# Kernel optimization log

Measured on AMD Instinct MI355X. Metric: run time of the kernel, lower is better.

The kernel has to match this reference:

```python
import jax, jax.numpy as jnp
import numpy as np

K = 20
EPS = 1e-5
NEG_SLOPE = 0.2


def knn_idx(x, k):
    # x: (B, C, N) -> idx: (B, N, k) of nearest neighbors by L2 distance
    inner = jnp.einsum('bcn,bcm->bnm', x, x)          # (B, N, N)
    xx = jnp.sum(x * x, axis=1)                        # (B, N)
    # negative squared distance: larger = closer
    neg_dist = 2.0 * inner - xx[:, :, None] - xx[:, None, :]
    _, idx = jax.lax.top_k(neg_dist, k)                # (B, N, k)
    return idx


def edge_feature(x, k):
    # x: (B, C, N) -> (B, 2C, N, k): concat(neighbor - x, x)
    idx = knn_idx(x, k)                                # (B, N, k)
    # neighbors[b,c,n,j] = x[b, c, idx[b,n,j]]
    nbr = jnp.take_along_axis(x[:, :, None, :], idx[:, None, :, :], axis=3)  # (B,C,N,k)
    xc = x[:, :, :, None]
    return jnp.concatenate([nbr - xc, jnp.broadcast_to(xc, nbr.shape)], axis=1)


def conv_bn_lrelu(h, W, gamma, beta):
    # 1x1 conv: h (B, Cin, N, k), W (Cout, Cin)
    h = jnp.einsum('oc,bcnk->bonk', W, h)
    # training-mode BatchNorm2d over (B, N, k) per channel
    mean = jnp.mean(h, axis=(0, 2, 3), keepdims=True)
    var = jnp.var(h, axis=(0, 2, 3), keepdims=True)
    h = (h - mean) * jax.lax.rsqrt(var + EPS)
    h = h * gamma[None, :, None, None] + beta[None, :, None, None]
    return jnp.where(h >= 0, h, NEG_SLOPE * h)


def setup_inputs() -> dict:
    key = jax.random.key(0)
    ks = jax.random.split(key, 3)
    B, C, N = 16, 3, 4096
    x = jax.random.normal(ks[0], (B, C, N), dtype=jnp.float32)
    W0 = jax.random.normal(ks[1], (64, 2 * C), dtype=jnp.float32) * (1.0 / np.sqrt(2 * C))
    W1 = jax.random.normal(ks[2], (64, 64), dtype=jnp.float32) * (1.0 / np.sqrt(64))
    g0 = jnp.ones((64,), jnp.float32); b0 = jnp.zeros((64,), jnp.float32)
    g1 = jnp.ones((64,), jnp.float32); b1 = jnp.zeros((64,), jnp.float32)
    return {"x": x, "W0": W0, "g0": g0, "b0": b0, "W1": W1, "g1": g1, "b1": b1}


def reference(x, W0, g0, b0, W1, g1, b1):
    h = edge_feature(x, K)                 # (B, 2C, N, k)
    h = conv_bn_lrelu(h, W0, g0, b0)       # (B, 64, N, k)
    h = conv_bn_lrelu(h, W1, g1, b1)       # (B, 64, N, k)
    return jnp.max(h, axis=-1)             # (B, 64, N)
```

## Files before the change

### kernel.cpp

```cpp
#include <hip/hip_runtime.h>
#include <cfloat>

#define NEG_SLOPE 0.2f
#define BN_EPS 1e-5f
#define EDGES 1310720
#define INV_M (1.0f / 1310720.0f)

typedef short v8s __attribute__((ext_vector_type(8)));
typedef float v4f __attribute__((ext_vector_type(4)));

__device__ __forceinline__ unsigned short f2bf(float f) {
  unsigned b = __float_as_uint(f);
  b += 0x7fffu + ((b >> 16) & 1u);
  return (unsigned short)(b >> 16);
}
__device__ __forceinline__ float bf2f(unsigned short s) {
  return __uint_as_float(((unsigned)s) << 16);
}

__device__ __forceinline__ float sqnorm_np(float c0, float c1, float c2) {
#pragma clang fp contract(off)
  return (c0 * c0 + c1 * c1) + c2 * c2;
}
__device__ __forceinline__ float negdist_np(float c0, float c1, float c2,
                                            float q0, float q1, float q2,
                                            float xxn, float xxm) {
#pragma clang fp contract(off)
  float inner = (c0 * q0 + c1 * q1) + c2 * q2;
  return (2.0f * inner - xxn) - xxm;
}

template <int PAT>
__device__ __forceinline__ float swzf(float v) {
  return __uint_as_float((unsigned)__builtin_amdgcn_ds_swizzle((int)__float_as_uint(v), PAT));
}
template <int PAT>
__device__ __forceinline__ int swzi(int v) {
  return __builtin_amdgcn_ds_swizzle(v, PAT);
}
__device__ __forceinline__ float bpermf(int addr, float v) {
  return __uint_as_float((unsigned)__builtin_amdgcn_ds_bpermute(addr, (int)__float_as_uint(v)));
}
__device__ __forceinline__ int bpermi(int addr, int v) {
  return __builtin_amdgcn_ds_bpermute(addr, v);
}
__device__ __forceinline__ int imin2(int a, int b) { return a < b ? a : b; }

__device__ __forceinline__ int pick_max(float v0, int i0, int xaddr) {
  float m = fmaxf(v0, swzf<0x041F>(v0));
  m = fmaxf(m, swzf<0x081F>(m));
  m = fmaxf(m, swzf<0x101F>(m));
  m = fmaxf(m, swzf<0x201F>(m));
  m = fmaxf(m, swzf<0x401F>(m));
  float vmax = fmaxf(m, bpermf(xaddr, m));
  unsigned long long mask = __ballot(v0 == vmax);
  if (__popcll(mask) == 1) {
    int L = (int)(__ffsll(mask) - 1);
    return __builtin_amdgcn_readlane(i0, L);
  }
  int t = (v0 == vmax) ? i0 : 0x7fffffff;
  t = imin2(t, swzi<0x041F>(t));
  t = imin2(t, swzi<0x081F>(t));
  t = imin2(t, swzi<0x101F>(t));
  t = imin2(t, swzi<0x201F>(t));
  t = imin2(t, swzi<0x401F>(t));
  t = imin2(t, bpermi(xaddr, t));
  return t;
}

__device__ __forceinline__ void ins3f(float nd, int m,
                                      float& v0, float& v1, float& v2,
                                      int& i0, int& i1, int& i2) {
  bool g0 = nd > v0, g1 = nd > v1, g2 = nd > v2;
  int ni2 = g2 ? (g1 ? i1 : m) : i2;
  int ni1 = g1 ? (g0 ? i0 : m) : i1;
  i0 = g0 ? m : i0;
  float nv1 = __builtin_amdgcn_fmed3f(nd, v0, v1);
  float nv2 = __builtin_amdgcn_fmed3f(nd, v1, v2);
  v0 = fmaxf(v0, nd);
  v1 = nv1; v2 = nv2; i1 = ni1; i2 = ni2;
}

__global__ __launch_bounds__(1024, 8) void k1_knn(const float* __restrict__ x, int* __restrict__ idxo) {
  __shared__ float4 xs[4096];
  int b   = blockIdx.x >> 5;
  int blk = blockIdx.x & 31;
  const float* xb = x + b * 12288;
  for (int i = threadIdx.x; i < 4096; i += 1024) {
    float a0 = xb[i], a1 = xb[4096 + i], a2 = xb[8192 + i];
    xs[i] = make_float4(a0, a1, a2, sqnorm_np(a0, a1, a2));
  }
  __syncthreads();

  int wv = threadIdx.x >> 6;
  int lane = threadIdx.x & 63;
  int wave_id = blk * 16 + wv;
  int xaddr = ((lane ^ 32) << 2);

  #pragma unroll 1
  for (int p = 0; p < 4; p++) {
    int nA = wave_id * 8 + 2 * p;
    int nB = nA + 1;
    float4 qA = xs[nA];
    float4 qB = xs[nB];

    float vA0 = -FLT_MAX, vA1 = -FLT_MAX, vA2 = -FLT_MAX;
    float vB0 = -FLT_MAX, vB1 = -FLT_MAX, vB2 = -FLT_MAX;
    int   iA0 = 0x7fffffff, iA1 = 0x7fffffff, iA2 = 0x7fffffff;
    int   iB0 = 0x7fffffff, iB1 = 0x7fffffff, iB2 = 0x7fffffff;
    #pragma unroll 2
    for (int j = 0; j < 64; j++) {
      int m = (j << 6) + lane;
      float4 c = xs[m];
      float ndA = negdist_np(c.x, c.y, c.z, qA.x, qA.y, qA.z, qA.w, c.w);
      ins3f(ndA, m, vA0, vA1, vA2, iA0, iA1, iA2);
      float ndB = negdist_np(c.x, c.y, c.z, qB.x, qB.y, qB.z, qB.w, c.w);
      ins3f(ndB, m, vB0, vB1, vB2, iB0, iB1, iB2);
    }

    unsigned long long remA = 0ull, remB = 0ull;
    int keepA = 0, keepB = 0;
    #pragma unroll 1
    for (int r = 0; r < 20; r++) {
      int winA = pick_max(vA0, iA0, xaddr);
      int winB = pick_max(vB0, iB0, xaddr);
      if (lane == r) { keepA = winA; keepB = winB; }

      bool ownA = ((winA & 63) == lane);
      remA |= ownA ? (1ull << (winA >> 6)) : 0ull;
      vA0 = ownA ? vA1 : vA0;  iA0 = ownA ? iA1 : iA0;
      vA1 = ownA ? vA2 : vA1;  iA1 = ownA ? iA2 : iA1;
      vA2 = ownA ? -FLT_MAX : vA2;  iA2 = ownA ? 0x7fffffff : iA2;
      if (ownA & (vA0 == -FLT_MAX)) {
        #pragma unroll 1
        for (int j = 0; j < 64; j++) {
          int m = (j << 6) + lane;
          float4 c = xs[m];
          float ndA = negdist_np(c.x, c.y, c.z, qA.x, qA.y, qA.z, qA.w, c.w);
          if ((remA >> j) & 1ull) ndA = -FLT_MAX;
          ins3f(ndA, m, vA0, vA1, vA2, iA0, iA1, iA2);
        }
      }
      bool ownB = ((winB & 63) == lane);
      remB |= ownB ? (1ull << (winB >> 6)) : 0ull;
      vB0 = ownB ? vB1 : vB0;  iB0 = ownB ? iB1 : iB0;
      vB1 = ownB ? vB2 : vB1;  iB1 = ownB ? iB2 : iB1;
      vB2 = ownB ? -FLT_MAX : vB2;  iB2 = ownB ? 0x7fffffff : iB2;
      if (ownB & (vB0 == -FLT_MAX)) {
        #pragma unroll 1
        for (int j = 0; j < 64; j++) {
          int m = (j << 6) + lane;
          float4 c = xs[m];
          float ndB = negdist_np(c.x, c.y, c.z, qB.x, qB.y, qB.z, qB.w, c.w);
          if ((remB >> j) & 1ull) ndB = -FLT_MAX;
          ins3f(ndB, m, vB0, vB1, vB2, iB0, iB1, iB2);
        }
      }
    }
    if (lane < 20) {
      idxo[((b << 12) + nA) * 20 + lane] = keepA;
      idxo[((b << 12) + nB) * 20 + lane] = keepB;
    }
  }
}

__global__ __launch_bounds__(256) void k2_moments(const float* __restrict__ x,
                                                  const int* __restrict__ idxi,
                                                  float* __restrict__ stat) {
  int P = blockIdx.x * 256 + threadIdx.x;
  int b = P >> 12, n = P & 4095;
  const float* xb = x + b * 12288;
  float xn0 = xb[n], xn1 = xb[4096 + n], xn2 = xb[8192 + n];
  const int* ip = idxi + P * 20;
  float Sd0 = 0.f, Sd1 = 0.f, Sd2 = 0.f;
  float S00 = 0.f, S01 = 0.f, S02 = 0.f, S11 = 0.f, S12 = 0.f, S22 = 0.f;
  #pragma unroll 4
  for (int j = 0; j < 20; j++) {
    int m = ip[j];
    float d0 = xb[m] - xn0, d1 = xb[4096 + m] - xn1, d2 = xb[8192 + m] - xn2;
    Sd0 += d0; Sd1 += d1; Sd2 += d2;
    S00 = fmaf(d0, d0, S00); S01 = fmaf(d0, d1, S01); S02 = fmaf(d0, d2, S02);
    S11 = fmaf(d1, d1, S11); S12 = fmaf(d1, d2, S12); S22 = fmaf(d2, d2, S22);
  }
  float acc[27];
  acc[0] = Sd0; acc[1] = Sd1; acc[2] = Sd2;
  acc[3] = 20.f * xn0; acc[4] = 20.f * xn1; acc[5] = 20.f * xn2;
  acc[6] = S00;  acc[7] = S01;  acc[8] = S02;
  acc[9] = Sd0 * xn0;  acc[10] = Sd0 * xn1; acc[11] = Sd0 * xn2;
  acc[12] = S11; acc[13] = S12;
  acc[14] = Sd1 * xn0; acc[15] = Sd1 * xn1; acc[16] = Sd1 * xn2;
  acc[17] = S22;
  acc[18] = Sd2 * xn0; acc[19] = Sd2 * xn1; acc[20] = Sd2 * xn2;
  acc[21] = 20.f * xn0 * xn0; acc[22] = 20.f * xn0 * xn1; acc[23] = 20.f * xn0 * xn2;
  acc[24] = 20.f * xn1 * xn1; acc[25] = 20.f * xn1 * xn2;
  acc[26] = 20.f * xn2 * xn2;
  #pragma unroll
  for (int i = 0; i < 27; i++) {
    float s = acc[i];
    for (int off = 32; off > 0; off >>= 1) s += __shfl_down(s, off);
    acc[i] = s;
  }
  __shared__ float red[4][27];
  int w = threadIdx.x >> 6, lane = threadIdx.x & 63;
  if (lane == 0) {
    #pragma unroll
    for (int i = 0; i < 27; i++) red[w][i] = acc[i];
  }
  __syncthreads();
  if (threadIdx.x < 27) {
    float s = red[0][threadIdx.x] + red[1][threadIdx.x] + red[2][threadIdx.x] + red[3][threadIdx.x];
    atomicAdd(&stat[threadIdx.x], s);
  }
}

__global__ __launch_bounds__(256) void k0_uv(const float* __restrict__ x, const float* __restrict__ W0,
                                             const float* __restrict__ stat,
                                             const float* __restrict__ g0v, const float* __restrict__ b0v,
                                             unsigned short* __restrict__ u, unsigned short* __restrict__ v) {
  int gid = blockIdx.x * 256 + threadIdx.x;
  int p = gid >> 6;
  int c = gid & 63;
  int b = p >> 12, n = p & 4095;

  float w[6];
  #pragma unroll
  for (int i = 0; i < 6; i++) w[i] = W0[c * 6 + i];
  float mean = 0.f;
  #pragma unroll
  for (int i = 0; i < 6; i++) mean += w[i] * stat[i];
  mean *= INV_M;
  float e2 = 0.f;
  int pp = 6;
  #pragma unroll
  for (int i = 0; i < 6; i++) {
    #pragma unroll
    for (int j = i; j < 6; j++) {
      float f = w[i] * w[j] * stat[pp]; pp++;
      e2 += (i == j) ? f : 2.f * f;
    }
  }
  e2 *= INV_M;
  float var = e2 - mean * mean;
  float a = g0v[c] * rsqrtf(var + BN_EPS);
  float bb = b0v[c] - mean * a;

  const float* xb = x + b * 12288;
  float x0 = xb[n], x1 = xb[4096 + n], x2 = xb[8192 + n];
  float uu = a * (w[0] * x0 + w[1] * x1 + w[2] * x2);
  float vv = a * ((w[3] - w[0]) * x0 + (w[4] - w[1]) * x1 + (w[5] - w[2]) * x2) + bb;
  u[gid] = f2bf(uu);
  v[gid] = f2bf(vv);
}

__global__ __launch_bounds__(256, 4) void k4_mfma(const unsigned short* __restrict__ u,
                                                  const unsigned short* __restrict__ v,
                                                  const int* __restrict__ idxi,
                                                  const float* __restrict__ W1,
                                                  float* __restrict__ psum,
                                                  unsigned short* __restrict__ maxb,
                                                  unsigned short* __restrict__ minb) {
  int lane = threadIdx.x & 63;
  int wv = threadIdx.x >> 6;
  int g = blockIdx.x * 4 + wv;
  int G = g * 16;
  int bbase = (G >> 12) << 12;
  int row16 = lane & 15;
  int quad = lane >> 4;

  v8s Bf[4][2];
  #pragma unroll
  for (int t = 0; t < 4; t++) {
    const float* wrow = W1 + (16 * t + row16) * 64 + quad * 8;
    #pragma unroll
    for (int kh = 0; kh < 2; kh++) {
      #pragma unroll
      for (int i = 0; i < 8; i++) Bf[t][kh][i] = (short)f2bf(wrow[kh * 32 + i]);
    }
  }
  const v8s* vrow = (const v8s*)(v + (G + row16) * 64);
  v8s vv0 = vrow[quad], vv1 = vrow[quad + 4];
  float v0f[8], v1f[8];
  #pragma unroll
  for (int i = 0; i < 8; i++) {
    v0f[i] = bf2f((unsigned short)vv0[i]);
    v1f[i] = bf2f((unsigned short)vv1[i]);
  }

  const int* ip = idxi + (G + row16) * 20;

  float mx[4][4], mn[4][4], s2a[4], sq2a[4];
  #pragma unroll
  for (int t = 0; t < 4; t++) {
    #pragma unroll
    for (int i = 0; i < 4; i++) { mx[t][i] = -FLT_MAX; mn[t][i] = FLT_MAX; }
    s2a[t] = 0.f; sq2a[t] = 0.f;
  }

  int m_next = ip[0];
  #pragma unroll 1
  for (int j = 0; j < 20; j++) {
    int m = bbase + m_next;
    if (j < 19) m_next = ip[j + 1];
    const v8s* urow = (const v8s*)(u + m * 64);
    v8s u0 = urow[quad], u1 = urow[quad + 4];
    v8s a0, a1f;
    #pragma unroll
    for (int i = 0; i < 8; i++) {
      float h = bf2f((unsigned short)u0[i]) + v0f[i];
      h = fmaxf(h, 0.2f * h);
      a0[i] = (short)f2bf(h);
      float h2 = bf2f((unsigned short)u1[i]) + v1f[i];
      h2 = fmaxf(h2, 0.2f * h2);
      a1f[i] = (short)f2bf(h2);
    }
    #pragma unroll
    for (int t = 0; t < 4; t++) {
      v4f c = {0.f, 0.f, 0.f, 0.f};
      c = __builtin_amdgcn_mfma_f32_16x16x32_bf16(a0, Bf[t][0], c, 0, 0, 0);
      c = __builtin_amdgcn_mfma_f32_16x16x32_bf16(a1f, Bf[t][1], c, 0, 0, 0);
      #pragma unroll
      for (int i = 0; i < 4; i++) {
        float cv = c[i];
        mx[t][i] = fmaxf(mx[t][i], cv);
        mn[t][i] = fminf(mn[t][i], cv);
        s2a[t] += cv;
        sq2a[t] = fmaf(cv, cv, sq2a[t]);
      }
    }
  }
  #pragma unroll
  for (int t = 0; t < 4; t++) {
    #pragma unroll
    for (int i = 0; i < 4; i++) {
      int P = G + quad * 4 + i;
      maxb[P * 64 + 16 * t + row16] = f2bf(mx[t][i]);
      minb[P * 64 + 16 * t + row16] = f2bf(mn[t][i]);
    }
  }
  #pragma unroll
  for (int t = 0; t < 4; t++) {
    float s = s2a[t], q = sq2a[t];
    s += __shfl_xor(s, 16); q += __shfl_xor(q, 16);
    s += __shfl_xor(s, 32); q += __shfl_xor(q, 32);
    if (quad == 0) {
      int c = 16 * t + row16;
      psum[c * 4096 + g] = s;
      psum[(64 + c) * 4096 + g] = q;
    }
  }
}

__global__ __launch_bounds__(256) void k4b_red(const float* __restrict__ psum, float* __restrict__ s2) {
  int c = blockIdx.x;
  const float* p = psum + c * 4096;
  float s = 0.f;
  for (int i = threadIdx.x; i < 4096; i += 256) s += p[i];
  for (int off = 32; off > 0; off >>= 1) s += __shfl_down(s, off);
  __shared__ float red[4];
  if ((threadIdx.x & 63) == 0) red[threadIdx.x >> 6] = s;
  __syncthreads();
  if (threadIdx.x == 0) s2[c] = red[0] + red[1] + red[2] + red[3];
}

__global__ __launch_bounds__(256) void k5_out(const unsigned short* __restrict__ maxb,
                                              const unsigned short* __restrict__ minb,
                                              const float* __restrict__ s2, const float* __restrict__ g1,
                                              const float* __restrict__ b1, float* __restrict__ out) {
  __shared__ float T[64][65];
  __shared__ float a2s[64], b2s[64];
  int blk = blockIdx.x;
  int b = blk >> 6;
  int n0 = (blk & 63) << 6;
  int t = threadIdx.x;
  if (t < 64) {
    float mean = s2[t] * INV_M;
    float var = s2[64 + t] * INV_M - mean * mean;
    float a = g1[t] * rsqrtf(var + BN_EPS);
    a2s[t] = a;
    b2s[t] = b1[t] - mean * a;
  }
  __syncthreads();
  #pragma unroll
  for (int i = 0; i < 16; i++) {
    int lin = i * 256 + t;
    int r = lin >> 6;
    int c = lin & 63;
    float a = a2s[c];
    int P = (b << 12) + n0 + r;
    float vfp = bf2f((a >= 0.f) ? maxb[P * 64 + c] : minb[P * 64 + c]);
    float z = a * vfp + b2s[c];
    T[c][r] = z >= 0.f ? z : NEG_SLOPE * z;
  }
  __syncthreads();
  #pragma unroll
  for (int i = 0; i < 16; i++) {
    int lin = i * 256 + t;
    int c = lin >> 6;
    int nn = lin & 63;
    out[(b * 64 + c) * 4096 + n0 + nn] = T[c][nn];
  }
}

extern "C" void kernel_launch(void* const* d_in, const int* in_sizes, int n_in,
                              void* d_out, int out_size, void* d_ws, size_t ws_size,
                              hipStream_t stream) {
  const float* x  = (const float*)d_in[0];
  const float* W0 = (const float*)d_in[1];
  const float* g0 = (const float*)d_in[2];
  const float* b0 = (const float*)d_in[3];
  const float* W1 = (const float*)d_in[4];
  const float* g1 = (const float*)d_in[5];
  const float* b1 = (const float*)d_in[6];
  float* out = (float*)d_out;
  char* ws = (char*)d_ws;

  int*            idx  = (int*)(ws + 0);
  float*          stat = (float*)(ws + 5242880);
  float*          s2   = (float*)(ws + 5242880 + 1024);
  float*          part = (float*)(ws + 5244416);
  unsigned short* u    = (unsigned short*)(ws + 7341568);
  unsigned short* v    = (unsigned short*)(ws + 15730176);
  unsigned short* maxb = (unsigned short*)(ws + 24118784);
  unsigned short* minb = (unsigned short*)(ws + 32507392);

  (void)hipMemsetAsync(stat, 0, 128, stream);
  k1_knn    <<<512, 1024, 0, stream>>>(x, idx);
  k2_moments<<<256, 256, 0, stream>>>(x, idx, stat);
  k0_uv     <<<16384, 256, 0, stream>>>(x, W0, stat, g0, b0, u, v);
  k4_mfma   <<<1024, 256, 0, stream>>>(u, v, idx, W1, part, maxb, minb);
  k4b_red   <<<128, 256, 0, stream>>>(part, s2);
  k5_out    <<<1024, 256, 0, stream>>>(maxb, minb, s2, g1, b1, out);
}
```

Baseline: 440.6 us.

## Process four queries per wave in kNN and prescale coordinates by two

The kNN kernel now handles four query points per pass instead of two, so each shared-memory candidate load is reused across more distance evaluations. Candidate coordinates are stored pre-doubled so the per-pair multiply by two disappears, with the queries halved to keep the distance values identical. Blocks shrink to 512 threads with twice as many blocks. The risks are higher register pressure from the larger per-query state and a changed occupancy balance.

```diff
diff --git a/kernel.cpp b/kernel.cpp
--- a/kernel.cpp
+++ b/kernel.cpp
@@ -22,12 +22,12 @@
 #pragma clang fp contract(off)
   return (c0 * c0 + c1 * c1) + c2 * c2;
 }
-__device__ __forceinline__ float negdist_np(float c0, float c1, float c2,
-                                            float q0, float q1, float q2,
-                                            float xxn, float xxm) {
+__device__ __forceinline__ float negdist2_np(float c0, float c1, float c2,
+                                             float q0, float q1, float q2,
+                                             float xxn, float xxm) {
 #pragma clang fp contract(off)
-  float inner = (c0 * q0 + c1 * q1) + c2 * q2;
-  return (2.0f * inner - xxn) - xxm;
+  float inner2 = (c0 * q0 + c1 * q1) + c2 * q2;
+  return (inner2 - xxn) - xxm;
 }
 
 template <int PAT>
@@ -81,85 +81,82 @@
   v1 = nv1; v2 = nv2; i1 = ni1; i2 = ni2;
 }
 
-__global__ __launch_bounds__(1024, 8) void k1_knn(const float* __restrict__ x, int* __restrict__ idxo) {
+__global__ __launch_bounds__(512, 4) void k1_knn(const float* __restrict__ x, int* __restrict__ idxo) {
   __shared__ float4 xs[4096];
-  int b   = blockIdx.x >> 5;
-  int blk = blockIdx.x & 31;
+  int b   = blockIdx.x >> 6;
+  int blk = blockIdx.x & 63;
   const float* xb = x + b * 12288;
-  for (int i = threadIdx.x; i < 4096; i += 1024) {
+  for (int i = threadIdx.x; i < 4096; i += 512) {
     float a0 = xb[i], a1 = xb[4096 + i], a2 = xb[8192 + i];
-    xs[i] = make_float4(a0, a1, a2, sqnorm_np(a0, a1, a2));
+    xs[i] = make_float4(2.0f * a0, 2.0f * a1, 2.0f * a2, sqnorm_np(a0, a1, a2));
   }
   __syncthreads();
 
   int wv = threadIdx.x >> 6;
   int lane = threadIdx.x & 63;
-  int wave_id = blk * 16 + wv;
+  int wave_id = blk * 8 + wv;
   int xaddr = ((lane ^ 32) << 2);
 
   #pragma unroll 1
-  for (int p = 0; p < 4; p++) {
-    int nA = wave_id * 8 + 2 * p;
-    int nB = nA + 1;
-    float4 qA = xs[nA];
-    float4 qB = xs[nB];
-
-    float vA0 = -FLT_MAX, vA1 = -FLT_MAX, vA2 = -FLT_MAX;
-    float vB0 = -FLT_MAX, vB1 = -FLT_MAX, vB2 = -FLT_MAX;
-    int   iA0 = 0x7fffffff, iA1 = 0x7fffffff, iA2 = 0x7fffffff;
-    int   iB0 = 0x7fffffff, iB1 = 0x7fffffff, iB2 = 0x7fffffff;
+  for (int s = 0; s < 2; s++) {
+    int nBase = wave_id * 8 + 4 * s;
+    float4 q[4];
+    #pragma unroll
+    for (int qi = 0; qi < 4; qi++) {
+      float4 raw = xs[nBase + qi];
+      q[qi].x = 0.5f * raw.x;
+      q[qi].y = 0.5f * raw.y;
+      q[qi].z = 0.5f * raw.z;
+      q[qi].w = raw.w;
+    }
+
+    float vv[4][3];
+    int   ii[4][3];
+    #pragma unroll
+    for (int qi = 0; qi < 4; qi++) {
+      vv[qi][0] = vv[qi][1] = vv[qi][2] = -FLT_MAX;
+      ii[qi][0] = ii[qi][1] = ii[qi][2] = 0x7fffffff;
+    }
+
     #pragma unroll 2
     for (int j = 0; j < 64; j++) {
       int m = (j << 6) + lane;
       float4 c = xs[m];
-      float ndA = negdist_np(c.x, c.y, c.z, qA.x, qA.y, qA.z, qA.w, c.w);
-      ins3f(ndA, m, vA0, vA1, vA2, iA0, iA1, iA2);
-      float ndB = negdist_np(c.x, c.y, c.z, qB.x, qB.y, qB.z, qB.w, c.w);
-      ins3f(ndB, m, vB0, vB1, vB2, iB0, iB1, iB2);
-    }
-
-    unsigned long long remA = 0ull, remB = 0ull;
-    int keepA = 0, keepB = 0;
+      #pragma unroll
+      for (int qi = 0; qi < 4; qi++) {
+        float nd = negdist2_np(c.x, c.y, c.z, q[qi].x, q[qi].y, q[qi].z, q[qi].w, c.w);
+        ins3f(nd, m, vv[qi][0], vv[qi][1], vv[qi][2], ii[qi][0], ii[qi][1], ii[qi][2]);
+      }
+    }
+
+    unsigned long long rem[4] = {0ull, 0ull, 0ull, 0ull};
+    int keep[4] = {0, 0, 0, 0};
     #pragma unroll 1
     for (int r = 0; r < 20; r++) {
-      int winA = pick_max(vA0, iA0, xaddr);
-      int winB = pick_max(vB0, iB0, xaddr);
-      if (lane == r) { keepA = winA; keepB = winB; }
-
-      bool ownA = ((winA & 63) == lane);
-      remA |= ownA ? (1ull << (winA >> 6)) : 0ull;
-      vA0 = ownA ? vA1 : vA0;  iA0 = ownA ? iA1 : iA0;
-      vA1 = ownA ? vA2 : vA1;  iA1 = ownA ? iA2 : iA1;
-      vA2 = ownA ? -FLT_MAX : vA2;  iA2 = ownA ? 0x7fffffff : iA2;
-      if (ownA & (vA0 == -FLT_MAX)) {
-        #pragma unroll 1
-        for (int j = 0; j < 64; j++) {
-          int m = (j << 6) + lane;
-          float4 c = xs[m];
-          float ndA = negdist_np(c.x, c.y, c.z, qA.x, qA.y, qA.z, qA.w, c.w);
-          if ((remA >> j) & 1ull) ndA = -FLT_MAX;
-          ins3f(ndA, m, vA0, vA1, vA2, iA0, iA1, iA2);
+      #pragma unroll
+      for (int qi = 0; qi < 4; qi++) {
+        int win = pick_max(vv[qi][0], ii[qi][0], xaddr);
+        if (lane == r) keep[qi] = win;
+        bool own = ((win & 63) == lane);
+        rem[qi] |= own ? (1ull << (win >> 6)) : 0ull;
+        vv[qi][0] = own ? vv[qi][1] : vv[qi][0];  ii[qi][0] = own ? ii[qi][1] : ii[qi][0];
+        vv[qi][1] = own ? vv[qi][2] : vv[qi][1];  ii[qi][1] = own ? ii[qi][2] : ii[qi][1];
+        vv[qi][2] = own ? -FLT_MAX : vv[qi][2];   ii[qi][2] = own ? 0x7fffffff : ii[qi][2];
+        if (own & (vv[qi][0] == -FLT_MAX)) {
+          #pragma unroll 1
+          for (int j = 0; j < 64; j++) {
+            int m = (j << 6) + lane;
+            float4 c = xs[m];
+            float nd = negdist2_np(c.x, c.y, c.z, q[qi].x, q[qi].y, q[qi].z, q[qi].w, c.w);
+            if ((rem[qi] >> j) & 1ull) nd = -FLT_MAX;
+            ins3f(nd, m, vv[qi][0], vv[qi][1], vv[qi][2], ii[qi][0], ii[qi][1], ii[qi][2]);
+          }
         }
       }
-      bool ownB = ((winB & 63) == lane);
-      remB |= ownB ? (1ull << (winB >> 6)) : 0ull;
-      vB0 = ownB ? vB1 : vB0;  iB0 = ownB ? iB1 : iB0;
-      vB1 = ownB ? vB2 : vB1;  iB1 = ownB ? iB2 : iB1;
-      vB2 = ownB ? -FLT_MAX : vB2;  iB2 = ownB ? 0x7fffffff : iB2;
-      if (ownB & (vB0 == -FLT_MAX)) {
-        #pragma unroll 1
-        for (int j = 0; j < 64; j++) {
-          int m = (j << 6) + lane;
-          float4 c = xs[m];
-          float ndB = negdist_np(c.x, c.y, c.z, qB.x, qB.y, qB.z, qB.w, c.w);
-          if ((remB >> j) & 1ull) ndB = -FLT_MAX;
-          ins3f(ndB, m, vB0, vB1, vB2, iB0, iB1, iB2);
-        }
-      }
-    }
-    if (lane < 20) {
-      idxo[((b << 12) + nA) * 20 + lane] = keepA;
-      idxo[((b << 12) + nB) * 20 + lane] = keepB;
+    }
+    #pragma unroll
+    for (int qi = 0; qi < 4; qi++) {
+      if (lane < 20) idxo[((b << 12) + nBase + qi) * 20 + lane] = keep[qi];
     }
   }
 }
@@ -424,7 +421,7 @@
   unsigned short* minb = (unsigned short*)(ws + 32507392);
 
   (void)hipMemsetAsync(stat, 0, 128, stream);
-  k1_knn    <<<512, 1024, 0, stream>>>(x, idx);
+  k1_knn    <<<1024, 512, 0, stream>>>(x, idx);
   k2_moments<<<256, 256, 0, stream>>>(x, idx, stat);
   k0_uv     <<<16384, 256, 0, stream>>>(x, W0, stat, g0, b0, u, v);
   k4_mfma   <<<1024, 256, 0, stream>>>(u, v, idx, W1, part, maxb, minb);
```

New measurement: 459.5 us. +4.3%, slower.
